# Kernel optimization log

Hardware: AMD Instinct MI355X
Metric: run time of the kernel (lower is better)

Reference implementation:

```python
import jax, jax.numpy as jnp
import numpy as np

QMAX = 127.0
QMIN = -128.0


def setup_inputs() -> dict:
    key = jax.random.key(0)
    k1, k2, k3 = jax.random.split(key, 3)
    B, N, D, O = 4, 4096, 2048, 2048
    x = jax.random.normal(k1, (B, N, D), dtype=jnp.float32)
    weight = jax.random.normal(k2, (O, D), dtype=jnp.float32)
    bias = jax.random.normal(k3, (O,), dtype=jnp.float32)
    return {"x": x, "weight": weight, "bias": bias}


def reference(x, weight, bias):
    # --- per-row symmetric int8 quantization of the weight [O, D] ---
    w_max = jnp.clip(jnp.max(jnp.abs(weight), axis=1, keepdims=True), 1e-8, None)
    w_scale = (w_max / QMAX)                     # [O, 1]
    w_q = jnp.clip(jnp.round(weight / w_scale), QMIN, QMAX).astype(jnp.int8)
    w_scale = w_scale.squeeze(1).astype(jnp.float32)  # [O]

    # --- dynamic per-row symmetric int8 quantization of x [B, N, D] ---
    x_max = jnp.max(jnp.abs(x), axis=2, keepdims=True)       # [B, N, 1]
    x_scale = jnp.maximum(x_max / QMAX, 1e-12)               # [B, N, 1]
    x_q = jnp.clip(jnp.round(x / x_scale), QMIN, QMAX).astype(jnp.int8)

    # --- int8 GEMM accumulated in int32: [B,N,D] x [O,D]^T -> [B,N,O] ---
    acc = jnp.einsum("bnd,od->bno", x_q.astype(jnp.int32), w_q.astype(jnp.int32))

    # --- dequantize with per-row activation scale and per-out-channel weight scale ---
    y = acc.astype(jnp.float32) * x_scale.astype(jnp.float32) * w_scale[None, None, :]
    y = y + bias
    return y.astype(x.dtype)
```

## Files before the change

kernel.cpp:

```cpp
#include <hip/hip_runtime.h>
#include <stdint.h>
#include <stddef.h>

typedef int v4i __attribute__((ext_vector_type(4)));

#define GLOAD_LDS16(g, l) __builtin_amdgcn_global_load_lds( \
    (const __attribute__((address_space(1))) void*)(g),     \
    (__attribute__((address_space(3))) void*)(l), 16, 0, 0)

__device__ __forceinline__ int pack4(float4 f, float s) {
    int a = (int)rintf(f.x / s); a = a < -128 ? -128 : (a > 127 ? 127 : a);
    int b = (int)rintf(f.y / s); b = b < -128 ? -128 : (b > 127 ? 127 : b);
    int c = (int)rintf(f.z / s); c = c < -128 ? -128 : (c > 127 ? 127 : c);
    int d = (int)rintf(f.w / s); d = d < -128 ? -128 : (d > 127 ? 127 : d);
    return (a & 255) | ((b & 255) << 8) | ((c & 255) << 16) | ((d & 255) << 24);
}

__global__ __launch_bounds__(256) void quant_rows_2048(
    const float* __restrict__ in, signed char* __restrict__ q,
    float* __restrict__ scales, float floorv)
{
    const int lane = threadIdx.x & 63;
    const int row  = blockIdx.x * 4 + (threadIdx.x >> 6);
    const float* rp = in + (size_t)row * 2048;

    float4 v[8];
#pragma unroll
    for (int j = 0; j < 2; ++j) {
        const float4* p = (const float4*)(rp + j * 1024 + lane * 16);
#pragma unroll
        for (int i = 0; i < 4; ++i) v[j * 4 + i] = p[i];
    }
    float am = 0.0f;
#pragma unroll
    for (int i = 0; i < 8; ++i) {
        am = fmaxf(am, fabsf(v[i].x));
        am = fmaxf(am, fabsf(v[i].y));
        am = fmaxf(am, fabsf(v[i].z));
        am = fmaxf(am, fabsf(v[i].w));
    }
#pragma unroll
    for (int off = 32; off; off >>= 1) am = fmaxf(am, __shfl_xor(am, off));
    const float s = fmaxf(am / 127.0f, floorv);

#pragma unroll
    for (int j = 0; j < 2; ++j) {
        int4 pk;
        pk.x = pack4(v[j * 4 + 0], s);
        pk.y = pack4(v[j * 4 + 1], s);
        pk.z = pack4(v[j * 4 + 2], s);
        pk.w = pack4(v[j * 4 + 3], s);
        *(int4*)(q + (size_t)row * 2048 + j * 1024 + lane * 16) = pk;
    }
    if (lane == 0) scales[row] = s;
}

__global__ __launch_bounds__(256) void quant_w_t(
    const float* __restrict__ in, signed char* __restrict__ qt,
    float* __restrict__ scales)
{
    const int lane = threadIdx.x & 63;
    const int row  = blockIdx.x * 4 + (threadIdx.x >> 6);
    const int f    = row >> 4;
    const int rl   = row & 15;
    const float* rp = in + (size_t)row * 2048;

    float4 v[8];
#pragma unroll
    for (int j = 0; j < 2; ++j) {
        const float4* p = (const float4*)(rp + j * 1024 + lane * 16);
#pragma unroll
        for (int i = 0; i < 4; ++i) v[j * 4 + i] = p[i];
    }
    float am = 0.0f;
#pragma unroll
    for (int i = 0; i < 8; ++i) {
        am = fmaxf(am, fabsf(v[i].x));
        am = fmaxf(am, fabsf(v[i].y));
        am = fmaxf(am, fabsf(v[i].z));
        am = fmaxf(am, fabsf(v[i].w));
    }
#pragma unroll
    for (int off = 32; off; off >>= 1) am = fmaxf(am, __shfl_xor(am, off));
    const float s = fmaxf(am / 127.0f, 1e-8f / 127.0f);

#pragma unroll
    for (int j = 0; j < 2; ++j) {
        int4 pk;
        pk.x = pack4(v[j * 4 + 0], s);
        pk.y = pack4(v[j * 4 + 1], s);
        pk.z = pack4(v[j * 4 + 2], s);
        pk.w = pack4(v[j * 4 + 3], s);
        const int kb  = j * 64 + lane;
        const int t   = kb >> 2;
        const int sub = kb & 3;
        *(int4*)(qt + (((size_t)(f * 32 + t)) << 10) + (rl << 4) + (sub << 8)) = pk;
    }
    if (lane == 0) scales[row] = s;
}

__global__ __launch_bounds__(512, 4) void gemm_i8_bt(
    const signed char* __restrict__ xq, const signed char* __restrict__ wqt,
    const float* __restrict__ xs, const float* __restrict__ ws,
    const float* __restrict__ bias, float* __restrict__ out, int K)
{
    __shared__ __align__(16) signed char lds[24576];

    const int tid  = threadIdx.x;
    const int lane = tid & 63;
    const int wid  = tid >> 6;
    const int wm   = wid >> 2;
    const int wn   = wid & 3;

    const int nwg  = gridDim.x * gridDim.y;
    int orig = blockIdx.y * gridDim.x + blockIdx.x;
    int swz  = ((nwg & 7) == 0) ? ((orig & 7) * (nwg >> 3) + (orig >> 3)) : orig;
    const int brow = (swz / gridDim.x) * 128;
    const int bcol = (swz % gridDim.x) * 256;

    const int gch  = (((tid & 3) ^ ((tid >> 3) & 3)) << 4);
    const int lofs = tid << 4;
    const signed char* gA = xq + (size_t)(brow + (tid >> 2)) * K;

#define BUFOFF(bb) ((bb) * 8192)
#define ST_A(tt, bb) GLOAD_LDS16(gA + (size_t)(tt) * 64 + gch, \
                                 lds + BUFOFF(bb) + lofs)

    const int rl   = lane & 15;
    const int ko   = lane >> 4;
    const int slot = ((ko ^ ((rl >> 1) & 3)) << 4);

#define FRAG_A(bb, r) (*(const v4i*)(lds + BUFOFF(bb) + (r) * 64 + slot))

    const int NTc = K >> 6;
    const signed char* gB = wqt + (((size_t)((bcol >> 4) + wn * 4) * NTc) << 10) + (lane << 4);
    const size_t bns = ((size_t)NTc) << 10;

    v4i acc[4][4] = {};
    const int ar = wm * 64 + rl;

    ST_A(0, 0);
    v4i bc0 = *(const v4i*)(gB);
    v4i bc1 = *(const v4i*)(gB + bns);
    v4i bc2 = *(const v4i*)(gB + 2 * bns);
    v4i bc3 = *(const v4i*)(gB + 3 * bns);
    ST_A(1, 1);
    asm volatile("s_waitcnt vmcnt(1)" ::: "memory");
    __builtin_amdgcn_s_barrier();

    const int NT = NTc;
    for (int t = 0; t < NT; ++t) {
        const int buf = t % 3;
        v4i bn0, bn1, bn2, bn3;
        if (t + 1 < NT) {
            const signed char* gBt = gB + ((size_t)(t + 1) << 10);
            bn0 = *(const v4i*)(gBt);
            bn1 = *(const v4i*)(gBt + bns);
            bn2 = *(const v4i*)(gBt + 2 * bns);
            bn3 = *(const v4i*)(gBt + 3 * bns);
        }
        if (t + 2 < NT) ST_A(t + 2, (t + 2) % 3);

        v4i af[4];
#pragma unroll
        for (int m = 0; m < 4; ++m) af[m] = FRAG_A(buf, ar + m * 16);
        __builtin_amdgcn_s_setprio(1);
#pragma unroll
        for (int m = 0; m < 4; ++m) {
            acc[m][0] = __builtin_amdgcn_mfma_i32_16x16x64_i8(af[m], bc0, acc[m][0], 0, 0, 0);
            acc[m][1] = __builtin_amdgcn_mfma_i32_16x16x64_i8(af[m], bc1, acc[m][1], 0, 0, 0);
            acc[m][2] = __builtin_amdgcn_mfma_i32_16x16x64_i8(af[m], bc2, acc[m][2], 0, 0, 0);
            acc[m][3] = __builtin_amdgcn_mfma_i32_16x16x64_i8(af[m], bc3, acc[m][3], 0, 0, 0);
        }
        __builtin_amdgcn_s_setprio(0);

        if (t + 2 < NT) {
            asm volatile("s_waitcnt vmcnt(1) lgkmcnt(0)" ::: "memory");
            __builtin_amdgcn_s_barrier();
        } else if (t + 1 < NT) {
            asm volatile("s_waitcnt vmcnt(0) lgkmcnt(0)" ::: "memory");
            __builtin_amdgcn_s_barrier();
        }
        bc0 = bn0; bc1 = bn1; bc2 = bn2; bc3 = bn3;
    }

    const int rg = lane >> 4;
#pragma unroll
    for (int n = 0; n < 4; ++n) {
        const int col = bcol + wn * 64 + n * 16 + rl;
        const float wsc = ws[col];
        const float bv  = bias[col];
#pragma unroll
        for (int m = 0; m < 4; ++m) {
#pragma unroll
            for (int j = 0; j < 4; ++j) {
                const int row = brow + wm * 64 + m * 16 + rg * 4 + j;
                out[(size_t)row * 2048 + col] =
                    (float)acc[m][n][j] * xs[row] * wsc + bv;
            }
        }
    }
#undef ST_A
#undef BUFOFF
#undef FRAG_A
}

extern "C" void kernel_launch(void* const* d_in, const int* in_sizes, int n_in,
                              void* d_out, int out_size, void* d_ws, size_t ws_size,
                              hipStream_t stream) {
    const float* x    = (const float*)d_in[0];
    const float* w    = (const float*)d_in[1];
    const float* bias = (const float*)d_in[2];
    float* out = (float*)d_out;

    const int D = 2048;
    const int O = in_sizes[2];
    const int M = in_sizes[0] / D;

    char* wsb = (char*)d_ws;
    signed char* xq  = (signed char*)wsb;
    signed char* wqt = (signed char*)(wsb + (size_t)M * D);
    float* xs  = (float*)(wsb + (size_t)M * D + (size_t)O * D);
    float* wsc = (float*)(wsb + (size_t)M * D + (size_t)O * D + (size_t)M * 4);

    quant_rows_2048<<<M / 4, 256, 0, stream>>>(x, xq, xs, 1e-12f);
    quant_w_t<<<O / 4, 256, 0, stream>>>(w, wqt, wsc);

    dim3 grid(O / 256, M / 128);
    gemm_i8_bt<<<grid, 512, 0, stream>>>(xq, wqt, xs, wsc, bias, out, D);
}
```

Baseline: 127.9 us.

## Switch int8 GEMM to 128x128 tiles with BK=128 per pipeline stage

The GEMM block tile changes from 128x256 with 8 waves to 128x128 with 4 waves. Each pipeline stage now covers a K-depth of 128, so each LDS stage holds 16KB of A with an 8-chunk XOR swizzle, and there are half as many barriers per K. B fragments for both 64-wide K halves are loaded directly from global at the start of each iteration, and split waitcnts let the second MFMA half overlap outstanding loads. The aim is to amortize barrier and sync overhead and deepen the K step. In exchange, each B tile is reused across fewer rows of the output, LDS use per block doubles, and B prefetch no longer spans iterations.

After: 124.5 us. 1.03x faster.

```diff
diff --git a/kernel.cpp b/kernel.cpp
--- a/kernel.cpp
+++ b/kernel.cpp
@@ -99,89 +99,110 @@
     if (lane == 0) scales[row] = s;
 }
 
-__global__ __launch_bounds__(512, 4) void gemm_i8_bt(
+__global__ __launch_bounds__(256, 3) void gemm_i8_bk128(
     const signed char* __restrict__ xq, const signed char* __restrict__ wqt,
     const float* __restrict__ xs, const float* __restrict__ ws,
     const float* __restrict__ bias, float* __restrict__ out, int K)
 {
-    __shared__ __align__(16) signed char lds[24576];
+    __shared__ __align__(16) signed char lds[49152];
 
     const int tid  = threadIdx.x;
     const int lane = tid & 63;
     const int wid  = tid >> 6;
-    const int wm   = wid >> 2;
-    const int wn   = wid & 3;
+    const int wm   = wid >> 1;
+    const int wn   = wid & 1;
 
     const int nwg  = gridDim.x * gridDim.y;
     int orig = blockIdx.y * gridDim.x + blockIdx.x;
     int swz  = ((nwg & 7) == 0) ? ((orig & 7) * (nwg >> 3) + (orig >> 3)) : orig;
     const int brow = (swz / gridDim.x) * 128;
-    const int bcol = (swz % gridDim.x) * 256;
-
-    const int gch  = (((tid & 3) ^ ((tid >> 3) & 3)) << 4);
-    const int lofs = tid << 4;
-    const signed char* gA = xq + (size_t)(brow + (tid >> 2)) * K;
-
-#define BUFOFF(bb) ((bb) * 8192)
-#define ST_A(tt, bb) GLOAD_LDS16(gA + (size_t)(tt) * 64 + gch, \
-                                 lds + BUFOFF(bb) + lofs)
-
-    const int rl   = lane & 15;
-    const int ko   = lane >> 4;
-    const int slot = ((ko ^ ((rl >> 1) & 3)) << 4);
-
-#define FRAG_A(bb, r) (*(const v4i*)(lds + BUFOFF(bb) + (r) * 64 + slot))
-
-    const int NTc = K >> 6;
-    const signed char* gB = wqt + (((size_t)((bcol >> 4) + wn * 4) * NTc) << 10) + (lane << 4);
-    const size_t bns = ((size_t)NTc) << 10;
+    const int bcol = (swz % gridDim.x) * 128;
+
+    const int gch = (((tid & 7) ^ ((tid >> 3) & 7)) << 4);
+    const signed char* gA = xq + (size_t)(brow + (tid >> 3)) * K;
+
+#define ST_A4(tt, bb) do {                                                                    \
+    GLOAD_LDS16(gA + (size_t)(tt) * 128 + gch,                      lds + (bb) * 16384 + (tid << 4));          \
+    GLOAD_LDS16(gA + (size_t)(32) * K + (size_t)(tt) * 128 + gch,   lds + (bb) * 16384 + 4096 + (tid << 4));   \
+    GLOAD_LDS16(gA + (size_t)(64) * K + (size_t)(tt) * 128 + gch,   lds + (bb) * 16384 + 8192 + (tid << 4));   \
+    GLOAD_LDS16(gA + (size_t)(96) * K + (size_t)(tt) * 128 + gch,   lds + (bb) * 16384 + 12288 + (tid << 4));  \
+} while (0)
+
+    const int rl = lane & 15;
+    const int ko = lane >> 4;
+    const int c0 = ((ko ^ (rl & 7)) << 4);
+    const int c1 = (((4 + ko) ^ (rl & 7)) << 4);
+
+#define FRAG_A(bb, r, cc) (*(const v4i*)(lds + (bb) * 16384 + (r) * 128 + (cc)))
+
+    const int NT64 = K >> 6;
+    const signed char* gB = wqt + (((size_t)((bcol >> 4) + wn * 4) * NT64) << 10) + (lane << 4);
+    const size_t bns = ((size_t)NT64) << 10;
 
     v4i acc[4][4] = {};
     const int ar = wm * 64 + rl;
 
-    ST_A(0, 0);
-    v4i bc0 = *(const v4i*)(gB);
-    v4i bc1 = *(const v4i*)(gB + bns);
-    v4i bc2 = *(const v4i*)(gB + 2 * bns);
-    v4i bc3 = *(const v4i*)(gB + 3 * bns);
-    ST_A(1, 1);
-    asm volatile("s_waitcnt vmcnt(1)" ::: "memory");
+    ST_A4(0, 0);
+    ST_A4(1, 1);
+    asm volatile("s_waitcnt vmcnt(4)" ::: "memory");
     __builtin_amdgcn_s_barrier();
 
-    const int NT = NTc;
+    const int NT = K >> 7;
     for (int t = 0; t < NT; ++t) {
         const int buf = t % 3;
-        v4i bn0, bn1, bn2, bn3;
-        if (t + 1 < NT) {
-            const signed char* gBt = gB + ((size_t)(t + 1) << 10);
-            bn0 = *(const v4i*)(gBt);
-            bn1 = *(const v4i*)(gBt + bns);
-            bn2 = *(const v4i*)(gBt + 2 * bns);
-            bn3 = *(const v4i*)(gBt + 3 * bns);
-        }
-        if (t + 2 < NT) ST_A(t + 2, (t + 2) % 3);
-
-        v4i af[4];
-#pragma unroll
-        for (int m = 0; m < 4; ++m) af[m] = FRAG_A(buf, ar + m * 16);
+        const bool st2 = (t + 2 < NT);
+
+        const signed char* gBt = gB + (((size_t)(2 * t)) << 10);
+        v4i bc0 = *(const v4i*)(gBt);
+        v4i bc1 = *(const v4i*)(gBt + bns);
+        v4i bc2 = *(const v4i*)(gBt + 2 * bns);
+        v4i bc3 = *(const v4i*)(gBt + 3 * bns);
+        v4i bn0 = *(const v4i*)(gBt + 1024);
+        v4i bn1 = *(const v4i*)(gBt + bns + 1024);
+        v4i bn2 = *(const v4i*)(gBt + 2 * bns + 1024);
+        v4i bn3 = *(const v4i*)(gBt + 3 * bns + 1024);
+        if (st2) ST_A4(t + 2, (t + 2) % 3);
+
+        v4i af0 = FRAG_A(buf, ar,      c0);
+        v4i af1 = FRAG_A(buf, ar + 16, c0);
+        v4i af2 = FRAG_A(buf, ar + 32, c0);
+        v4i af3 = FRAG_A(buf, ar + 48, c0);
+        v4i an0 = FRAG_A(buf, ar,      c1);
+        v4i an1 = FRAG_A(buf, ar + 16, c1);
+        v4i an2 = FRAG_A(buf, ar + 32, c1);
+        v4i an3 = FRAG_A(buf, ar + 48, c1);
+
+        if (st2) asm volatile("s_waitcnt vmcnt(8) lgkmcnt(4)" ::: "memory");
+        else     asm volatile("s_waitcnt vmcnt(4) lgkmcnt(4)" ::: "memory");
+        __builtin_amdgcn_sched_barrier(0);
+
         __builtin_amdgcn_s_setprio(1);
 #pragma unroll
         for (int m = 0; m < 4; ++m) {
-            acc[m][0] = __builtin_amdgcn_mfma_i32_16x16x64_i8(af[m], bc0, acc[m][0], 0, 0, 0);
-            acc[m][1] = __builtin_amdgcn_mfma_i32_16x16x64_i8(af[m], bc1, acc[m][1], 0, 0, 0);
-            acc[m][2] = __builtin_amdgcn_mfma_i32_16x16x64_i8(af[m], bc2, acc[m][2], 0, 0, 0);
-            acc[m][3] = __builtin_amdgcn_mfma_i32_16x16x64_i8(af[m], bc3, acc[m][3], 0, 0, 0);
+            v4i a = (m == 0) ? af0 : (m == 1) ? af1 : (m == 2) ? af2 : af3;
+            acc[m][0] = __builtin_amdgcn_mfma_i32_16x16x64_i8(a, bc0, acc[m][0], 0, 0, 0);
+            acc[m][1] = __builtin_amdgcn_mfma_i32_16x16x64_i8(a, bc1, acc[m][1], 0, 0, 0);
+            acc[m][2] = __builtin_amdgcn_mfma_i32_16x16x64_i8(a, bc2, acc[m][2], 0, 0, 0);
+            acc[m][3] = __builtin_amdgcn_mfma_i32_16x16x64_i8(a, bc3, acc[m][3], 0, 0, 0);
         }
         __builtin_amdgcn_s_setprio(0);
 
-        if (t + 2 < NT) {
-            asm volatile("s_waitcnt vmcnt(1) lgkmcnt(0)" ::: "memory");
-            __builtin_amdgcn_s_barrier();
-        } else if (t + 1 < NT) {
-            asm volatile("s_waitcnt vmcnt(0) lgkmcnt(0)" ::: "memory");
-            __builtin_amdgcn_s_barrier();
+        if (st2) asm volatile("s_waitcnt vmcnt(4) lgkmcnt(0)" ::: "memory");
+        else     asm volatile("s_waitcnt vmcnt(0) lgkmcnt(0)" ::: "memory");
+        __builtin_amdgcn_sched_barrier(0);
+
+        __builtin_amdgcn_s_setprio(1);
+#pragma unroll
+        for (int m = 0; m < 4; ++m) {
+            v4i a = (m == 0) ? an0 : (m == 1) ? an1 : (m == 2) ? an2 : an3;
+            acc[m][0] = __builtin_amdgcn_mfma_i32_16x16x64_i8(a, bn0, acc[m][0], 0, 0, 0);
+            acc[m][1] = __builtin_amdgcn_mfma_i32_16x16x64_i8(a, bn1, acc[m][1], 0, 0, 0);
+            acc[m][2] = __builtin_amdgcn_mfma_i32_16x16x64_i8(a, bn2, acc[m][2], 0, 0, 0);
+            acc[m][3] = __builtin_amdgcn_mfma_i32_16x16x64_i8(a, bn3, acc[m][3], 0, 0, 0);
         }
-        bc0 = bn0; bc1 = bn1; bc2 = bn2; bc3 = bn3;
+        __builtin_amdgcn_s_setprio(0);
+
+        __builtin_amdgcn_s_barrier();
     }
 
     const int rg = lane >> 4;
@@ -200,8 +221,7 @@
             }
         }
     }
-#undef ST_A
-#undef BUFOFF
+#undef ST_A4
 #undef FRAG_A
 }
 
@@ -226,6 +246,6 @@
     quant_rows_2048<<<M / 4, 256, 0, stream>>>(x, xq, xs, 1e-12f);
     quant_w_t<<<O / 4, 256, 0, stream>>>(w, wqt, wsc);
 
-    dim3 grid(O / 256, M / 128);
-    gemm_i8_bt<<<grid, 512, 0, stream>>>(xq, wqt, xs, wsc, bias, out, D);
-}
+    dim3 grid(O / 128, M / 128);
+    gemm_i8_bk128<<<grid, 256, 0, stream>>>(xq, wqt, xs, wsc, bias, out, D);
+}
```

## Enlarge GEMM tile to 256x256 with K=128 steps and staged LDS loads

Applied to the files above, without the earlier changes.

Doubles the M tile per workgroup to 256 rows and the K step to 128, so each warp holds 8x4 accumulators and B fragments are reused across twice as many rows. A-tile loads are split into four sub-stages interleaved with four MFMA phases separated by barriers, using a larger 96KB triple-buffered LDS with an 8-way XOR swizzle. This cuts global B traffic per output and amortizes loop overhead, at the cost of lower occupancy (launch bounds 2), more registers, and extra barriers per iteration.

Measured after the change: 140.1 us. 1.1x slower.

```diff
diff --git a/kernel.cpp b/kernel.cpp
--- a/kernel.cpp
+++ b/kernel.cpp
@@ -99,12 +99,12 @@
     if (lane == 0) scales[row] = s;
 }
 
-__global__ __launch_bounds__(512, 4) void gemm_i8_bt(
+__global__ __launch_bounds__(512, 2) void gemm_i8_m201(
     const signed char* __restrict__ xq, const signed char* __restrict__ wqt,
     const float* __restrict__ xs, const float* __restrict__ ws,
     const float* __restrict__ bias, float* __restrict__ out, int K)
 {
-    __shared__ __align__(16) signed char lds[24576];
+    __shared__ __align__(16) signed char lds[98304];
 
     const int tid  = threadIdx.x;
     const int lane = tid & 63;
@@ -115,73 +115,108 @@
     const int nwg  = gridDim.x * gridDim.y;
     int orig = blockIdx.y * gridDim.x + blockIdx.x;
     int swz  = ((nwg & 7) == 0) ? ((orig & 7) * (nwg >> 3) + (orig >> 3)) : orig;
-    const int brow = (swz / gridDim.x) * 128;
+    const int brow = (swz / gridDim.x) * 256;
     const int bcol = (swz % gridDim.x) * 256;
 
-    const int gch  = (((tid & 3) ^ ((tid >> 3) & 3)) << 4);
-    const int lofs = tid << 4;
-    const signed char* gA = xq + (size_t)(brow + (tid >> 2)) * K;
-
-#define BUFOFF(bb) ((bb) * 8192)
-#define ST_A(tt, bb) GLOAD_LDS16(gA + (size_t)(tt) * 64 + gch, \
-                                 lds + BUFOFF(bb) + lofs)
-
-    const int rl   = lane & 15;
-    const int ko   = lane >> 4;
-    const int slot = ((ko ^ ((rl >> 1) & 3)) << 4);
-
-#define FRAG_A(bb, r) (*(const v4i*)(lds + BUFOFF(bb) + (r) * 64 + slot))
-
-    const int NTc = K >> 6;
-    const signed char* gB = wqt + (((size_t)((bcol >> 4) + wn * 4) * NTc) << 10) + (lane << 4);
-    const size_t bns = ((size_t)NTc) << 10;
-
-    v4i acc[4][4] = {};
-    const int ar = wm * 64 + rl;
-
-    ST_A(0, 0);
-    v4i bc0 = *(const v4i*)(gB);
-    v4i bc1 = *(const v4i*)(gB + bns);
-    v4i bc2 = *(const v4i*)(gB + 2 * bns);
-    v4i bc3 = *(const v4i*)(gB + 3 * bns);
-    ST_A(1, 1);
-    asm volatile("s_waitcnt vmcnt(1)" ::: "memory");
-    __builtin_amdgcn_s_barrier();
-
-    const int NT = NTc;
+    const int gch = (((tid & 7) ^ ((tid >> 3) & 7)) << 4);
+    const signed char* gA = xq + (size_t)(brow + (tid >> 3)) * K;
+
+#define ST_A(tt, bb, s) GLOAD_LDS16(                                          \
+    gA + (size_t)(64 * (s)) * K + (size_t)(tt) * 128 + gch,                   \
+    lds + (bb) * 32768 + (s) * 8192 + (tid << 4))
+
+    const int rl = lane & 15;
+    const int ko = lane >> 4;
+
+#define FRAG_A(bb, r, q) (*(const v4i*)(lds + (bb) * 32768 + (r) * 128 + \
+                                        ((((q) ^ ((r) & 7))) << 4)))
+
+    const int NT64 = K >> 6;
+    const signed char* gB = wqt + (((size_t)((bcol >> 4) + wn * 4) * NT64) << 10) + (lane << 4);
+    const size_t bns = ((size_t)NT64) << 10;
+
+    v4i acc[8][4] = {};
+    const int ar = wm * 128 + rl;
+
+#define MFMA16(MB, KS)                                                                     \
+    do {                                                                                   \
+        __builtin_amdgcn_s_setprio(1);                                                     \
+        _Pragma("unroll")                                                                  \
+        for (int mm = 0; mm < 4; ++mm) {                                                   \
+            acc[MB + mm][0] = __builtin_amdgcn_mfma_i32_16x16x64_i8(af[mm], bc[KS*4+0], acc[MB + mm][0], 0, 0, 0); \
+            acc[MB + mm][1] = __builtin_amdgcn_mfma_i32_16x16x64_i8(af[mm], bc[KS*4+1], acc[MB + mm][1], 0, 0, 0); \
+            acc[MB + mm][2] = __builtin_amdgcn_mfma_i32_16x16x64_i8(af[mm], bc[KS*4+2], acc[MB + mm][2], 0, 0, 0); \
+            acc[MB + mm][3] = __builtin_amdgcn_mfma_i32_16x16x64_i8(af[mm], bc[KS*4+3], acc[MB + mm][3], 0, 0, 0); \
+        }                                                                                  \
+        __builtin_amdgcn_s_setprio(0);                                                     \
+    } while (0)
+
+#define BAR()  __builtin_amdgcn_s_barrier()
+#define LGKM0() do { asm volatile("s_waitcnt lgkmcnt(0)" ::: "memory"); \
+                     __builtin_amdgcn_sched_barrier(0); } while (0)
+
+    ST_A(0, 0, 0); ST_A(0, 0, 1); ST_A(0, 0, 2); ST_A(0, 0, 3);
+    ST_A(1, 1, 0); ST_A(1, 1, 1); ST_A(1, 1, 2); ST_A(1, 1, 3);
+    asm volatile("s_waitcnt vmcnt(4)" ::: "memory");
+    BAR();
+
+    const int NT = K >> 7;
     for (int t = 0; t < NT; ++t) {
         const int buf = t % 3;
-        v4i bn0, bn1, bn2, bn3;
-        if (t + 1 < NT) {
-            const signed char* gBt = gB + ((size_t)(t + 1) << 10);
-            bn0 = *(const v4i*)(gBt);
-            bn1 = *(const v4i*)(gBt + bns);
-            bn2 = *(const v4i*)(gBt + 2 * bns);
-            bn3 = *(const v4i*)(gBt + 3 * bns);
+        const int nb  = (t + 2) % 3;
+        const bool st = (t + 2 < NT);
+        v4i af[4], bc[8];
+
+        af[0] = FRAG_A(buf, ar,      ko);
+        af[1] = FRAG_A(buf, ar + 16, ko);
+        af[2] = FRAG_A(buf, ar + 32, ko);
+        af[3] = FRAG_A(buf, ar + 48, ko);
+        {
+            const signed char* gBt = gB + (((size_t)(2 * t)) << 10);
+#pragma unroll
+            for (int n = 0; n < 4; ++n) {
+                bc[n]     = *(const v4i*)(gBt + n * bns);
+                bc[4 + n] = *(const v4i*)(gBt + n * bns + 1024);
+            }
         }
-        if (t + 2 < NT) ST_A(t + 2, (t + 2) % 3);
-
-        v4i af[4];
-#pragma unroll
-        for (int m = 0; m < 4; ++m) af[m] = FRAG_A(buf, ar + m * 16);
-        __builtin_amdgcn_s_setprio(1);
-#pragma unroll
-        for (int m = 0; m < 4; ++m) {
-            acc[m][0] = __builtin_amdgcn_mfma_i32_16x16x64_i8(af[m], bc0, acc[m][0], 0, 0, 0);
-            acc[m][1] = __builtin_amdgcn_mfma_i32_16x16x64_i8(af[m], bc1, acc[m][1], 0, 0, 0);
-            acc[m][2] = __builtin_amdgcn_mfma_i32_16x16x64_i8(af[m], bc2, acc[m][2], 0, 0, 0);
-            acc[m][3] = __builtin_amdgcn_mfma_i32_16x16x64_i8(af[m], bc3, acc[m][3], 0, 0, 0);
+        if (st) ST_A(t + 2, nb, 0);
+        BAR(); LGKM0();
+        MFMA16(0, 0);
+        BAR();
+
+        af[0] = FRAG_A(buf, ar + 64,  ko);
+        af[1] = FRAG_A(buf, ar + 80,  ko);
+        af[2] = FRAG_A(buf, ar + 96,  ko);
+        af[3] = FRAG_A(buf, ar + 112, ko);
+        if (st) ST_A(t + 2, nb, 1);
+        BAR(); LGKM0();
+        MFMA16(4, 0);
+        BAR();
+
+        af[0] = FRAG_A(buf, ar,      4 + ko);
+        af[1] = FRAG_A(buf, ar + 16, 4 + ko);
+        af[2] = FRAG_A(buf, ar + 32, 4 + ko);
+        af[3] = FRAG_A(buf, ar + 48, 4 + ko);
+        if (st) ST_A(t + 2, nb, 2);
+        BAR(); LGKM0();
+        MFMA16(0, 1);
+        BAR();
+
+        af[0] = FRAG_A(buf, ar + 64,  4 + ko);
+        af[1] = FRAG_A(buf, ar + 80,  4 + ko);
+        af[2] = FRAG_A(buf, ar + 96,  4 + ko);
+        af[3] = FRAG_A(buf, ar + 112, 4 + ko);
+        if (st) ST_A(t + 2, nb, 3);
+        BAR(); LGKM0();
+        MFMA16(4, 1);
+
+        if (t + 2 < NT) {
+            asm volatile("s_waitcnt vmcnt(4)" ::: "memory");
+            BAR();
+        } else if (t + 2 == NT) {
+            asm volatile("s_waitcnt vmcnt(0)" ::: "memory");
+            BAR();
         }
-        __builtin_amdgcn_s_setprio(0);
-
-        if (t + 2 < NT) {
-            asm volatile("s_waitcnt vmcnt(1) lgkmcnt(0)" ::: "memory");
-            __builtin_amdgcn_s_barrier();
-        } else if (t + 1 < NT) {
-            asm volatile("s_waitcnt vmcnt(0) lgkmcnt(0)" ::: "memory");
-            __builtin_amdgcn_s_barrier();
-        }
-        bc0 = bn0; bc1 = bn1; bc2 = bn2; bc3 = bn3;
     }
 
     const int rg = lane >> 4;
@@ -191,18 +226,20 @@
         const float wsc = ws[col];
         const float bv  = bias[col];
 #pragma unroll
-        for (int m = 0; m < 4; ++m) {
+        for (int m = 0; m < 8; ++m) {
 #pragma unroll
             for (int j = 0; j < 4; ++j) {
-                const int row = brow + wm * 64 + m * 16 + rg * 4 + j;
+                const int row = brow + wm * 128 + m * 16 + rg * 4 + j;
                 out[(size_t)row * 2048 + col] =
                     (float)acc[m][n][j] * xs[row] * wsc + bv;
             }
         }
     }
 #undef ST_A
-#undef BUFOFF
 #undef FRAG_A
+#undef MFMA16
+#undef BAR
+#undef LGKM0
 }
 
 extern "C" void kernel_launch(void* const* d_in, const int* in_sizes, int n_in,
@@ -226,6 +263,6 @@
     quant_rows_2048<<<M / 4, 256, 0, stream>>>(x, xq, xs, 1e-12f);
     quant_w_t<<<O / 4, 256, 0, stream>>>(w, wqt, wsc);
 
-    dim3 grid(O / 256, M / 128);
-    gemm_i8_bt<<<grid, 512, 0, stream>>>(xq, wqt, xs, wsc, bias, out, D);
-}
+    dim3 grid(O / 256, M / 256);
+    gemm_i8_m201<<<grid, 512, 0, stream>>>(xq, wqt, xs, wsc, bias, out, D);
+}
```
